# Performance work log

Hardware: AMD Instinct MI355X
Metric: run time of the kernel (lower is better)

## Reference

```python
import jax, jax.numpy as jnp
import numpy as np
from jax.ops import segment_sum, segment_max

N = 20000   # nodes per node type (glom, imm)
E = 320000  # edges per edge type (avg degree 16)
D = 256     # feature dim (in == out, required by GIN's (1+eps)*x + aggr)
LN_EPS = 1e-5


def _ln_relu(x, gamma, beta):
    mu = jnp.mean(x, axis=-1, keepdims=True)
    var = jnp.mean((x - mu) ** 2, axis=-1, keepdims=True)
    return jax.nn.relu((x - mu) * jax.lax.rsqrt(var + LN_EPS) * gamma + beta)


def _forward(x_glom, x_imm, ew_gg, ea_ig, W_gcn, b_gcn, Wl, bl, Wr, br, att, We,
             b_gat, eps, W_gin, b_gin, gamma, beta, ei_gg, ei_ig, ei_gi):
    # ---- GCNConv on (glom->glom): add_self_loops=True, edge_weight=ew_gg ----
    src, dst = ei_gg[0], ei_gg[1]
    xw = x_glom @ W_gcn                                   # [N, D]
    deg = segment_sum(ew_gg, dst, num_segments=N) + 1.0   # +1 for self-loop weight
    dinv = jax.lax.rsqrt(deg)                             # [N]
    coef = dinv[src] * ew_gg * dinv[dst]                  # [E] symmetric gcn_norm
    out_gcn = segment_sum(coef[:, None] * xw[src], dst, num_segments=N)
    out_gcn = out_gcn + (dinv * dinv)[:, None] * xw + b_gcn  # self-loop + bias

    # ---- GATv2Conv on (imm->glom): heads=1, edge_dim=1, no self loops ----
    s, d = ei_ig[0], ei_ig[1]
    hl = x_imm @ Wl + bl          # lin_l on source  [N, D]
    hr = x_glom @ Wr + br         # lin_r on target  [N, D]
    he = ea_ig @ We               # lin_edge         [E, D]
    z = jax.nn.leaky_relu(hl[s] + hr[d] + he, 0.2)
    logits = z @ att              # [E]
    m = segment_max(logits, d, num_segments=N)            # stable segment softmax
    ex = jnp.exp(logits - m[d])
    denom = segment_sum(ex, d, num_segments=N)
    alpha = ex / denom[d]
    out_gat = segment_sum(alpha[:, None] * hl[s], d, num_segments=N) + b_gat

    # ---- GINConv on (glom->imm): nn = Linear, train_eps ----
    s2, d2 = ei_gi[0], ei_gi[1]
    agg = segment_sum(x_glom[s2], d2, num_segments=N)     # sum aggregation
    out_gin = ((1.0 + eps[0]) * x_imm + agg) @ W_gin + b_gin

    # HeteroConv(aggr='sum') across edge types per destination node type,
    # then shared LayerNorm + ReLU
    glom = _ln_relu(out_gcn + out_gat, gamma, beta)
    imm = _ln_relu(out_gin, gamma, beta)
    return glom, imm


def setup_inputs() -> dict:
    key = jax.random.key(0)
    k = jax.random.split(key, 13)
    s = 0.06  # ~ glorot-ish scale for D=256
    return {
        'x_glom': jax.random.normal(k[0], (N, D), jnp.float32),
        'x_imm': jax.random.normal(k[1], (N, D), jnp.float32),
        'ew_gg': jax.random.uniform(k[2], (E,), jnp.float32),
        'ea_ig': jax.random.normal(k[3], (E, 1), jnp.float32),
        'W_gcn': jax.random.normal(k[4], (D, D), jnp.float32) * s,
        'b_gcn': jnp.zeros((D,), jnp.float32),
        'Wl': jax.random.normal(k[5], (D, D), jnp.float32) * s,
        'bl': jnp.zeros((D,), jnp.float32),
        'Wr': jax.random.normal(k[6], (D, D), jnp.float32) * s,
        'br': jnp.zeros((D,), jnp.float32),
        'att': jax.random.normal(k[7], (D,), jnp.float32) * s,
        'We': jax.random.normal(k[8], (1, D), jnp.float32) * s,
        'b_gat': jnp.zeros((D,), jnp.float32),
        'eps': jnp.zeros((1,), jnp.float32),
        'W_gin': jax.random.normal(k[9], (D, D), jnp.float32) * s,
        'b_gin': jnp.zeros((D,), jnp.float32),
        'gamma': jnp.ones((D,), jnp.float32),
        'beta': jnp.zeros((D,), jnp.float32),
        'ei_gg': jax.random.randint(k[10], (2, E), 0, N),
        'ei_ig': jax.random.randint(k[11], (2, E), 0, N),
        'ei_gi': jax.random.randint(k[12], (2, E), 0, N),
    }


def reference(x_glom, x_imm, ew_gg, ea_ig, W_gcn, b_gcn, Wl, bl, Wr, br, att, We,
              b_gat, eps, W_gin, b_gin, gamma, beta, ei_gg, ei_ig, ei_gi):
    return _forward(x_glom, x_imm, ew_gg, ea_ig, W_gcn, b_gcn, Wl, bl, Wr, br,
                    att, We, b_gat, eps, W_gin, b_gin, gamma, beta,
                    ei_gg, ei_ig, ei_gi)
```

## Files before the change

### kernel.cpp

```cpp
#include <hip/hip_runtime.h>


constexpr int D = 256;

typedef __attribute__((ext_vector_type(4))) float f32x4v;
typedef __attribute__((ext_vector_type(8))) short short8;

__device__ __forceinline__ float4 ld4(const float* p) {
    return *reinterpret_cast<const float4*>(p);
}
__device__ __forceinline__ void st4(float* p, float4 v) {
    *reinterpret_cast<float4*>(p) = v;
}
__device__ __forceinline__ unsigned short f2bf(float f) {
    unsigned u = __float_as_uint(f);
    u = u + 0x7FFFu + ((u >> 16) & 1u);
    return (unsigned short)(u >> 16);
}
__device__ __forceinline__ float bf2f(unsigned short u) {
    return __uint_as_float(((unsigned)u) << 16);
}
__device__ __forceinline__ float4 ldb4(const unsigned short* p) {
    ushort4 u = *reinterpret_cast<const ushort4*>(p);
    return make_float4(bf2f(u.x), bf2f(u.y), bf2f(u.z), bf2f(u.w));
}
__device__ __forceinline__ float wave_sum(float p) {
#pragma unroll
    for (int off = 32; off > 0; off >>= 1) p += __shfl_xor(p, off, 64);
    return p;
}
__device__ __forceinline__ float gat_partial(float4 h, float4 hrv, float ea,
                                             float4 We4, float4 att4) {
    float z, pp = 0.f;
    z = h.x + hrv.x + ea * We4.x; z *= (z > 0.f) ? 1.0f : 0.2f; pp += z * att4.x;
    z = h.y + hrv.y + ea * We4.y; z *= (z > 0.f) ? 1.0f : 0.2f; pp += z * att4.y;
    z = h.z + hrv.z + ea * We4.z; z *= (z > 0.f) ? 1.0f : 0.2f; pp += z * att4.z;
    z = h.w + hrv.w + ea * We4.w; z *= (z > 0.f) ? 1.0f : 0.2f; pp += z * att4.w;
    return pp;
}

__global__ void k_cast2(const float* __restrict__ x0, unsigned short* __restrict__ y0,
                        const float* __restrict__ x1, unsigned short* __restrict__ y1,
                        int n4)
{
    int i = blockIdx.x * 256 + threadIdx.x;
    if (i >= n4) return;
    const float* x = blockIdx.y ? x1 : x0;
    unsigned short* y = blockIdx.y ? y1 : y0;
    float4 v = ld4(x + (size_t)i * 4);
    ushort4 o;
    o.x = f2bf(v.x); o.y = f2bf(v.y); o.z = f2bf(v.z); o.w = f2bf(v.w);
    *reinterpret_cast<ushort4*>(y + (size_t)i * 4) = o;
}

__global__ void k_prep_wtz(const float* __restrict__ W0, const float* __restrict__ W1,
                           const float* __restrict__ W2, const float* __restrict__ W3,
                           unsigned short* __restrict__ Wt, int* __restrict__ counts,
                           float* __restrict__ deg, int n3, int N)
{
    int w = blockIdx.y;
    int i = blockIdx.x * 256 + threadIdx.x;
    if (w < 4) {
        const float* W = (w == 0) ? W0 : (w == 1) ? W1 : (w == 2) ? W2 : W3;
        int c = i >> 8, k = i & 255;
        Wt[(size_t)w * D * D + i] = f2bf(W[k * D + c]);
    } else {
        if (i < n3) counts[i] = 0;
        if (i < N) deg[i] = 1.0f;
    }
}

__global__ __launch_bounds__(256)
void k_proj(const unsigned short* __restrict__ xbg,
            const unsigned short* __restrict__ xbi,
            const unsigned short* __restrict__ Wt,
            const float* __restrict__ deg,
            const float* __restrict__ br, const float* __restrict__ bl,
            unsigned short* __restrict__ xws, unsigned short* __restrict__ hr,
            unsigned short* __restrict__ hl, int M)
{
    const int lane = threadIdx.x & 63;
    const int wave = threadIdx.x >> 6;
    const int lr = lane & 15;
    const int lk = lane >> 4;
    const int yy = blockIdx.y;
    const int row0 = blockIdx.x * 256 + wave * 64;

    const unsigned short* A;
    const unsigned short* Bt0;
    int col0;
    if (yy < 8) { A = xbg; Bt0 = Wt;             col0 = yy * 64; }
    else        { A = xbi; Bt0 = Wt + 2 * D * D; col0 = (yy - 8) * 64; }

    const unsigned short* ap[4];
#pragma unroll
    for (int rf = 0; rf < 4; ++rf) {
        int arow = row0 + rf * 16 + lr;
        int arow_c = (arow < M) ? arow : (M - 1);
        ap[rf] = A + (size_t)arow_c * D + lk * 8;
    }
    const unsigned short* bp = Bt0 + (size_t)(col0 + lr) * D + lk * 8;

    f32x4v acc[4][4] = {};
#pragma unroll
    for (int k0 = 0; k0 < 256; k0 += 32) {
        short8 af[4], bf[4];
#pragma unroll
        for (int rf = 0; rf < 4; ++rf)
            af[rf] = *reinterpret_cast<const short8*>(ap[rf] + k0);
#pragma unroll
        for (int nf = 0; nf < 4; ++nf)
            bf[nf] = *reinterpret_cast<const short8*>(bp + (size_t)nf * 16 * D + k0);
#pragma unroll
        for (int rf = 0; rf < 4; ++rf)
#pragma unroll
            for (int nf = 0; nf < 4; ++nf)
                acc[rf][nf] = __builtin_amdgcn_mfma_f32_16x16x32_bf16(
                    af[rf], bf[nf], acc[rf][nf], 0, 0, 0);
    }

#pragma unroll
    for (int nf = 0; nf < 4; ++nf) {
        int c = col0 + nf * 16 + lr;
        unsigned short* dst;
        int cc;
        float bv;
        bool scaled;
        if (yy < 8) {
            if (c < 256) { dst = xws; cc = c;       bv = 0.f;    scaled = true;  }
            else         { dst = hr;  cc = c - 256; bv = br[cc]; scaled = false; }
        } else           { dst = hl;  cc = c;       bv = bl[cc]; scaled = false; }
#pragma unroll
        for (int rf = 0; rf < 4; ++rf) {
#pragma unroll
            for (int i = 0; i < 4; ++i) {
                int r = row0 + rf * 16 + 4 * lk + i;
                if (r < M) {
                    float sc = scaled ? rsqrtf(deg[r]) : 1.0f;
                    dst[(size_t)r * D + cc] = f2bf(acc[rf][nf][i] * sc + bv);
                }
            }
        }
    }
}

__global__ __launch_bounds__(256)
void k_gin_gemm_ln(const unsigned short* __restrict__ A,
                   const unsigned short* __restrict__ Bt,
                   const float* __restrict__ bias,
                   const float* __restrict__ gamma, const float* __restrict__ beta,
                   float* __restrict__ out, int M)
{
    __shared__ float lds_s[4][64];
    __shared__ float lds_q[4][64];
    const int lane = threadIdx.x & 63;
    const int wave = threadIdx.x >> 6;
    const int lr = lane & 15;
    const int lk = lane >> 4;
    const int row0 = blockIdx.x * 64;
    const int col0 = wave * 64;

    const unsigned short* ap[4];
#pragma unroll
    for (int rf = 0; rf < 4; ++rf) {
        int arow = row0 + rf * 16 + lr;
        int arow_c = (arow < M) ? arow : (M - 1);
        ap[rf] = A + (size_t)arow_c * D + lk * 8;
    }
    const unsigned short* bp = Bt + (size_t)(col0 + lr) * D + lk * 8;

    f32x4v acc[4][4] = {};
#pragma unroll
    for (int k0 = 0; k0 < 256; k0 += 32) {
        short8 af[4], bf[4];
#pragma unroll
        for (int rf = 0; rf < 4; ++rf)
            af[rf] = *reinterpret_cast<const short8*>(ap[rf] + k0);
#pragma unroll
        for (int nf = 0; nf < 4; ++nf)
            bf[nf] = *reinterpret_cast<const short8*>(bp + (size_t)nf * 16 * D + k0);
#pragma unroll
        for (int rf = 0; rf < 4; ++rf)
#pragma unroll
            for (int nf = 0; nf < 4; ++nf)
                acc[rf][nf] = __builtin_amdgcn_mfma_f32_16x16x32_bf16(
                    af[rf], bf[nf], acc[rf][nf], 0, 0, 0);
    }

    float bv[4], gv[4], be[4];
#pragma unroll
    for (int nf = 0; nf < 4; ++nf) {
        int c = col0 + nf * 16 + lr;
        bv[nf] = bias[c]; gv[nf] = gamma[c]; be[nf] = beta[c];
    }

#pragma unroll
    for (int rf = 0; rf < 4; ++rf) {
        float ps[4], pq[4];
#pragma unroll
        for (int i = 0; i < 4; ++i) {
            float s = 0.f, q = 0.f;
#pragma unroll
            for (int nf = 0; nf < 4; ++nf) {
                float v = acc[rf][nf][i] + bv[nf];
                acc[rf][nf][i] = v;
                s += v; q += v * v;
            }
            ps[i] = s; pq[i] = q;
        }
#pragma unroll
        for (int off = 1; off < 16; off <<= 1) {
#pragma unroll
            for (int i = 0; i < 4; ++i) {
                ps[i] += __shfl_xor(ps[i], off, 64);
                pq[i] += __shfl_xor(pq[i], off, 64);
            }
        }
        if (lr == 0) {
#pragma unroll
            for (int i = 0; i < 4; ++i) {
                lds_s[wave][rf * 16 + lk * 4 + i] = ps[i];
                lds_q[wave][rf * 16 + lk * 4 + i] = pq[i];
            }
        }
    }
    __syncthreads();

#pragma unroll
    for (int rf = 0; rf < 4; ++rf) {
#pragma unroll
        for (int i = 0; i < 4; ++i) {
            int rl = rf * 16 + 4 * lk + i;
            float s = lds_s[0][rl] + lds_s[1][rl] + lds_s[2][rl] + lds_s[3][rl];
            float q = lds_q[0][rl] + lds_q[1][rl] + lds_q[2][rl] + lds_q[3][rl];
            float mu  = s * (1.0f / 256.0f);
            float var = q * (1.0f / 256.0f) - mu * mu;
            float rs  = rsqrtf(var + 1e-5f);
            int r = row0 + rl;
            if (r < M) {
#pragma unroll
                for (int nf = 0; nf < 4; ++nf) {
                    out[(size_t)r * D + col0 + nf * 16 + lr] =
                        fmaxf(0.f, (acc[rf][nf][i] - mu) * rs * gv[nf] + be[nf]);
                }
            }
        }
    }
}

__global__ void k_hist3(const int* __restrict__ ei_gg, const int* __restrict__ ei_ig,
                        const int* __restrict__ ei_gi, const float* __restrict__ ew_gg,
                        int* __restrict__ counts, int* __restrict__ rank,
                        float* __restrict__ deg, int E, int N)
{
    int e = blockIdx.x * 256 + threadIdx.x;
    if (e >= E) return;
    int t = blockIdx.y;
    const int* ei = (t == 0) ? ei_gg : (t == 1) ? ei_ig : ei_gi;
    int d = ei[E + e];
    rank[(size_t)t * E + e] = atomicAdd(&counts[t * N + d], 1);
    if (t == 0) atomicAdd(&deg[d], ew_gg[e]);
}

__global__ __launch_bounds__(256)
void k_scan_tile(const int* __restrict__ counts, int* __restrict__ rows,
                 int* __restrict__ partials, int N, int TPT)
{
    int t = blockIdx.y, tile = blockIdx.x;
    int i = tile * 256 + threadIdx.x;
    __shared__ int sh[256];
    int v = (i < N) ? counts[(size_t)t * N + i] : 0;
    sh[threadIdx.x] = v;
    __syncthreads();
#pragma unroll
    for (int off = 1; off < 256; off <<= 1) {
        int add = (threadIdx.x >= off) ? sh[threadIdx.x - off] : 0;
        __syncthreads();
        sh[threadIdx.x] += add;
        __syncthreads();
    }
    if (i < N) rows[(size_t)t * (N + 1) + i] = sh[threadIdx.x] - v;
    if (threadIdx.x == 255) partials[t * TPT + tile] = sh[255];
}

__global__ __launch_bounds__(128)
void k_scan_part(int* __restrict__ partials, int TPT)
{
    int t = blockIdx.x;
    __shared__ int sh[128];
    int v = (threadIdx.x < TPT) ? partials[t * TPT + threadIdx.x] : 0;
    sh[threadIdx.x] = v;
    __syncthreads();
#pragma unroll
    for (int off = 1; off < 128; off <<= 1) {
        int add = (threadIdx.x >= off) ? sh[threadIdx.x - off] : 0;
        __syncthreads();
        sh[threadIdx.x] += add;
        __syncthreads();
    }
    if (threadIdx.x < TPT) partials[t * TPT + threadIdx.x] = sh[threadIdx.x] - v;
}

__global__ void k_scan_final(int* __restrict__ rows, const int* __restrict__ partials,
                             int N, int TPT, int E)
{
    int i = blockIdx.x * 256 + threadIdx.x;
    if (i >= 3 * N) return;
    int t = i / N, j = i - t * N;
    rows[(size_t)t * (N + 1) + j] += partials[t * TPT + (j >> 8)];
    if (j == 0) rows[(size_t)t * (N + 1) + N] = E;
}

__global__ void k_scatter3(const int* __restrict__ ei_gg, const int* __restrict__ ei_ig,
                           const int* __restrict__ ei_gi, const float* __restrict__ ew_gg,
                           const float* __restrict__ ea_ig,
                           const int* __restrict__ rows, const int* __restrict__ rank,
                           int2* __restrict__ pk_gcn, int2* __restrict__ pk_gat,
                           int* __restrict__ src_gin, int E, int N)
{
    int e = blockIdx.x * 256 + threadIdx.x;
    if (e >= E) return;
    int t = blockIdx.y;
    if (t == 0) {
        int s = ei_gg[e], d = ei_gg[E + e];
        int pos = rows[d] + rank[e];
        pk_gcn[pos] = make_int2(s, __float_as_int(ew_gg[e]));
    } else if (t == 1) {
        int s = ei_ig[e], d = ei_ig[E + e];
        int pos = rows[(N + 1) + d] + rank[(size_t)E + e];
        pk_gat[pos] = make_int2(s, __float_as_int(ea_ig[e]));
    } else {
        int s = ei_gi[e], d = ei_gi[E + e];
        int pos = rows[2 * (N + 1) + d] + rank[2 * (size_t)E + e];
        src_gin[pos] = s;
    }
}

__global__ __launch_bounds__(256)
void k_gather_fused(const unsigned short* __restrict__ xws,
                    const unsigned short* __restrict__ hl,
                    const unsigned short* __restrict__ hr,
                    const float* __restrict__ deg,
                    const int* __restrict__ rows_gcn, const int2* __restrict__ pk_gcn,
                    const int* __restrict__ rows_gat, const int2* __restrict__ pk_gat,
                    const float* __restrict__ We, const float* __restrict__ att,
                    const float* __restrict__ b_gcn, const float* __restrict__ b_gat,
                    const float* __restrict__ gamma, const float* __restrict__ beta,
                    float* __restrict__ glom_out,
                    const unsigned short* __restrict__ xb_glom,
                    const float* __restrict__ x_imm, const float* __restrict__ eps,
                    const int* __restrict__ rows_gin, const int* __restrict__ src_gin,
                    unsigned short* __restrict__ agg,
                    int N)
{
    int gw   = __builtin_amdgcn_readfirstlane((blockIdx.x * 256 + threadIdx.x) >> 6);
    int lane = threadIdx.x & 63;

    if (gw < N) {
        int node = gw;
        float4 We4  = ld4(&We[lane * 4]);
        float4 att4 = ld4(&att[lane * 4]);
        float4 hrv  = ldb4(&hr[(size_t)node * D + lane * 4]);

        float di = rsqrtf(deg[node]);
        float4 acc = ldb4(&xws[(size_t)node * D + lane * 4]);
        float4 g0  = ld4(&b_gcn[lane * 4]);
        float4 a0  = ld4(&b_gat[lane * 4]);
        acc.x = di * acc.x + g0.x + a0.x;
        acc.y = di * acc.y + g0.y + a0.y;
        acc.z = di * acc.z + g0.z + a0.z;
        acc.w = di * acc.w + g0.w + a0.w;

        int p  = rows_gcn[node];
        int p1 = rows_gcn[node + 1];
        for (; p + 4 <= p1; p += 4) {
            int2  pk[4];
            float cf[4];
            float4 v[4];
#pragma unroll
            for (int j = 0; j < 4; ++j) pk[j] = pk_gcn[p + j];
#pragma unroll
            for (int j = 0; j < 4; ++j) cf[j] = __int_as_float(pk[j].y) * di;
#pragma unroll
            for (int j = 0; j < 4; ++j) v[j] = ldb4(&xws[(size_t)pk[j].x * D + lane * 4]);
#pragma unroll
            for (int j = 0; j < 4; ++j) {
                acc.x += cf[j] * v[j].x; acc.y += cf[j] * v[j].y;
                acc.z += cf[j] * v[j].z; acc.w += cf[j] * v[j].w;
            }
        }
        for (; p < p1; ++p) {
            int2 pk = pk_gcn[p];
            float cx = __int_as_float(pk.y) * di;
            float4 v = ldb4(&xws[(size_t)pk.x * D + lane * 4]);
            acc.x += cx * v.x; acc.y += cx * v.y;
            acc.z += cx * v.z; acc.w += cx * v.w;
        }

        int q  = rows_gat[node];
        int q1 = rows_gat[node + 1];
        int has = (q1 > q);
        float m = -3.4e38f, den = 0.f;
        float4 ag = make_float4(0.f, 0.f, 0.f, 0.f);
        for (; q + 4 <= q1; q += 4) {
            int2  pk[4];
            float4 h[4];
            float pp[4];
#pragma unroll
            for (int j = 0; j < 4; ++j) pk[j] = pk_gat[q + j];
#pragma unroll
            for (int j = 0; j < 4; ++j) h[j] = ldb4(&hl[(size_t)pk[j].x * D + lane * 4]);
#pragma unroll
            for (int j = 0; j < 4; ++j)
                pp[j] = wave_sum(gat_partial(h[j], hrv, __int_as_float(pk[j].y), We4, att4));
            float mb = fmaxf(fmaxf(pp[0], pp[1]), fmaxf(pp[2], pp[3]));
            float mn = fmaxf(m, mb);
            float scale = __expf(m - mn);
            float x[4];
#pragma unroll
            for (int j = 0; j < 4; ++j) x[j] = __expf(pp[j] - mn);
            den = den * scale + (x[0] + x[1]) + (x[2] + x[3]);
            float axx = 0.f, ayy = 0.f, azz = 0.f, aww = 0.f;
#pragma unroll
            for (int j = 0; j < 4; ++j) {
                axx += x[j] * h[j].x; ayy += x[j] * h[j].y;
                azz += x[j] * h[j].z; aww += x[j] * h[j].w;
            }
            ag.x = ag.x * scale + axx; ag.y = ag.y * scale + ayy;
            ag.z = ag.z * scale + azz; ag.w = ag.w * scale + aww;
            m = mn;
        }
        for (; q < q1; ++q) {
            int2 pk = pk_gat[q];
            float4 h = ldb4(&hl[(size_t)pk.x * D + lane * 4]);
            float pp = wave_sum(gat_partial(h, hrv, __int_as_float(pk.y), We4, att4));
            float mn = fmaxf(m, pp);
            float scale = __expf(m - mn);
            float ex = __expf(pp - mn);
            den = den * scale + ex;
            ag.x = ag.x * scale + ex * h.x;
            ag.y = ag.y * scale + ex * h.y;
            ag.z = ag.z * scale + ex * h.z;
            ag.w = ag.w * scale + ex * h.w;
            m = mn;
        }
        if (has) {
            float inv = 1.0f / den;
            acc.x += ag.x * inv; acc.y += ag.y * inv;
            acc.z += ag.z * inv; acc.w += ag.w * inv;
        }

        float s_ = acc.x + acc.y + acc.z + acc.w;
        float sq = acc.x * acc.x + acc.y * acc.y + acc.z * acc.z + acc.w * acc.w;
#pragma unroll
        for (int off = 32; off > 0; off >>= 1) {
            s_ += __shfl_xor(s_, off, 64);
            sq += __shfl_xor(sq, off, 64);
        }
        float mu  = s_ * (1.0f / 256.0f);
        float var = sq * (1.0f / 256.0f) - mu * mu;
        float rs  = rsqrtf(var + 1e-5f);
        float4 g = ld4(&gamma[lane * 4]);
        float4 b = ld4(&beta[lane * 4]);
        float4 o;
        o.x = fmaxf(0.f, (acc.x - mu) * rs * g.x + b.x);
        o.y = fmaxf(0.f, (acc.y - mu) * rs * g.y + b.y);
        o.z = fmaxf(0.f, (acc.z - mu) * rs * g.z + b.z);
        o.w = fmaxf(0.f, (acc.w - mu) * rs * g.w + b.w);
        st4(&glom_out[(size_t)node * D + lane * 4], o);
    } else if (gw < 2 * N) {
        int node = gw - N;
        float c = 1.0f + eps[0];
        float4 acc = ld4(&x_imm[(size_t)node * D + lane * 4]);
        acc.x *= c; acc.y *= c; acc.z *= c; acc.w *= c;
        int p  = rows_gin[node];
        int p1 = rows_gin[node + 1];
        for (; p + 4 <= p1; p += 4) {
            int s[4];
            float4 v[4];
#pragma unroll
            for (int j = 0; j < 4; ++j) s[j] = src_gin[p + j];
#pragma unroll
            for (int j = 0; j < 4; ++j) v[j] = ldb4(&xb_glom[(size_t)s[j] * D + lane * 4]);
            acc.x += (v[0].x + v[1].x) + (v[2].x + v[3].x);
            acc.y += (v[0].y + v[1].y) + (v[2].y + v[3].y);
            acc.z += (v[0].z + v[1].z) + (v[2].z + v[3].z);
            acc.w += (v[0].w + v[1].w) + (v[2].w + v[3].w);
        }
        for (; p < p1; ++p) {
            int sx = src_gin[p];
            float4 v = ldb4(&xb_glom[(size_t)sx * D + lane * 4]);
            acc.x += v.x; acc.y += v.y; acc.z += v.z; acc.w += v.w;
        }
        ushort4 o;
        o.x = f2bf(acc.x); o.y = f2bf(acc.y); o.z = f2bf(acc.z); o.w = f2bf(acc.w);
        *reinterpret_cast<ushort4*>(agg + (size_t)node * D + lane * 4) = o;
    }
}

extern "C" void kernel_launch(void* const* d_in, const int* in_sizes, int n_in,
                              void* d_out, int out_size, void* d_ws, size_t ws_size,
                              hipStream_t stream)
{
    const float* x_glom = (const float*)d_in[0];
    const float* x_imm  = (const float*)d_in[1];
    const float* ew_gg  = (const float*)d_in[2];
    const float* ea_ig  = (const float*)d_in[3];
    const float* W_gcn  = (const float*)d_in[4];
    const float* b_gcn  = (const float*)d_in[5];
    const float* Wl     = (const float*)d_in[6];
    const float* bl     = (const float*)d_in[7];
    const float* Wr     = (const float*)d_in[8];
    const float* br     = (const float*)d_in[9];
    const float* att    = (const float*)d_in[10];
    const float* We     = (const float*)d_in[11];
    const float* b_gat  = (const float*)d_in[12];
    const float* eps    = (const float*)d_in[13];
    const float* W_gin  = (const float*)d_in[14];
    const float* b_gin  = (const float*)d_in[15];
    const float* gamma  = (const float*)d_in[16];
    const float* beta   = (const float*)d_in[17];
    const int*   ei_gg  = (const int*)d_in[18];
    const int*   ei_ig  = (const int*)d_in[19];
    const int*   ei_gi  = (const int*)d_in[20];

    const int N = in_sizes[0] / D;
    const int E = in_sizes[2];
    const size_t ND = (size_t)N * D;
    const int TPT = (N + 255) / 256;

    char* base = (char*)d_ws;
    size_t off = 0;
    auto alloc = [&](size_t bytes) {
        void* p = base + off;
        off = (off + bytes + 255) & ~(size_t)255;
        return p;
    };
    unsigned short* xb_glom = (unsigned short*)alloc(ND * 2);
    unsigned short* xb_imm  = (unsigned short*)alloc(ND * 2);
    unsigned short* xws_b   = (unsigned short*)alloc(ND * 2);
    unsigned short* hl_b    = (unsigned short*)alloc(ND * 2);
    unsigned short* hr_b    = (unsigned short*)alloc(ND * 2);
    unsigned short* agg_b   = (unsigned short*)alloc(ND * 2);
    unsigned short* Wt      = (unsigned short*)alloc(4 * D * D * 2);
    float* deg     = (float*)alloc(N * 4);
    int*   counts  = (int*)alloc(3 * (size_t)N * 4);
    int*   rows    = (int*)alloc(3 * (size_t)(N + 1) * 4);
    int*   parts   = (int*)alloc(3 * (size_t)TPT * 4);
    int*   rank    = (int*)alloc(3 * (size_t)E * 4);
    int2*  pk_gcn  = (int2*)alloc((size_t)E * 8);
    int2*  pk_gat  = (int2*)alloc((size_t)E * 8);
    int*   src_gin = (int*)alloc((size_t)E * 4);

    float* glom_out = (float*)d_out;
    float* imm_out  = (float*)d_out + ND;

    int nb_cast  = (int)((ND / 4 + 255) / 256);
    int nb_3n    = (3 * N + 255) / 256;
    int nb_e     = (E + 255) / 256;
    int nb_2nw   = (2 * N + 3) / 4;

    k_cast2<<<dim3(nb_cast, 2), 256, 0, stream>>>(x_glom, xb_glom, x_imm, xb_imm,
                                                  (int)(ND / 4));
    k_prep_wtz<<<dim3(256, 5), 256, 0, stream>>>(W_gcn, Wr, Wl, W_gin, Wt,
                                                 counts, deg, 3 * N, N);
    k_hist3<<<dim3(nb_e, 3), 256, 0, stream>>>(ei_gg, ei_ig, ei_gi, ew_gg,
                                               counts, rank, deg, E, N);
    k_scan_tile<<<dim3(TPT, 3), 256, 0, stream>>>(counts, rows, parts, N, TPT);
    k_scan_part<<<3, 128, 0, stream>>>(parts, TPT);
    k_scan_final<<<nb_3n, 256, 0, stream>>>(rows, parts, N, TPT, E);
    k_scatter3<<<dim3(nb_e, 3), 256, 0, stream>>>(ei_gg, ei_ig, ei_gi, ew_gg, ea_ig,
                                                  rows, rank, pk_gcn, pk_gat,
                                                  src_gin, E, N);
    k_proj<<<dim3((N + 255) / 256, 12), 256, 0, stream>>>(
        xb_glom, xb_imm, Wt, deg, br, bl, xws_b, hr_b, hl_b, N);
    k_gather_fused<<<nb_2nw, 256, 0, stream>>>(
        xws_b, hl_b, hr_b, deg,
        rows, pk_gcn,
        rows + (N + 1), pk_gat,
        We, att, b_gcn, b_gat, gamma, beta, glom_out,
        xb_glom, x_imm, eps,
        rows + 2 * (N + 1), src_gin, agg_b, N);
    k_gin_gemm_ln<<<(N + 63) / 64, 256, 0, stream>>>(
        agg_b, Wt + 3 * D * D, b_gin, gamma, beta, imm_out, N);
}
```

Before: 250.3 us.

## Merge front-end and projection/scatter kernels, memset counters, prefetch edge indices

Merges the cast, weight transpose and histogram kernels into one launch, and the projection GEMM and CSR scatter into another. This cuts the number of kernel launches and lets independent work run concurrently. The counter and degree init becomes a memset, and the degree is stored as a sum with the +1 applied at use. The gather loops now software-prefetch the next four edge records to hide index-load latency, at the cost of a few more registers.

Result: faster. 240.4 us (-3.9%).

```diff
diff --git a/kernel.cpp b/kernel.cpp
--- a/kernel.cpp
+++ b/kernel.cpp
@@ -39,227 +39,51 @@
     return pp;
 }
 
-__global__ void k_cast2(const float* __restrict__ x0, unsigned short* __restrict__ y0,
-                        const float* __restrict__ x1, unsigned short* __restrict__ y1,
-                        int n4)
-{
-    int i = blockIdx.x * 256 + threadIdx.x;
-    if (i >= n4) return;
-    const float* x = blockIdx.y ? x1 : x0;
-    unsigned short* y = blockIdx.y ? y1 : y0;
-    float4 v = ld4(x + (size_t)i * 4);
-    ushort4 o;
-    o.x = f2bf(v.x); o.y = f2bf(v.y); o.z = f2bf(v.z); o.w = f2bf(v.w);
-    *reinterpret_cast<ushort4*>(y + (size_t)i * 4) = o;
-}
-
-__global__ void k_prep_wtz(const float* __restrict__ W0, const float* __restrict__ W1,
-                           const float* __restrict__ W2, const float* __restrict__ W3,
-                           unsigned short* __restrict__ Wt, int* __restrict__ counts,
-                           float* __restrict__ deg, int n3, int N)
-{
-    int w = blockIdx.y;
-    int i = blockIdx.x * 256 + threadIdx.x;
-    if (w < 4) {
+__global__ __launch_bounds__(256)
+void k_front(const float* __restrict__ x_glom, const float* __restrict__ x_imm,
+             unsigned short* __restrict__ xb_glom, unsigned short* __restrict__ xb_imm,
+             const float* __restrict__ W0, const float* __restrict__ W1,
+             const float* __restrict__ W2, const float* __restrict__ W3,
+             unsigned short* __restrict__ Wt,
+             const int* __restrict__ ei_gg, const int* __restrict__ ei_ig,
+             const int* __restrict__ ei_gi, const float* __restrict__ ew_gg,
+             int* __restrict__ counts, int* __restrict__ rank,
+             float* __restrict__ degsum,
+             int n4, int nbCast, int nbHist, int E, int N)
+{
+    int bx = blockIdx.x;
+    if (bx < 2 * nbCast) {
+        bool second = (bx >= nbCast);
+        int i = (second ? bx - nbCast : bx) * 256 + threadIdx.x;
+        if (i < n4) {
+            const float* x = second ? x_imm : x_glom;
+            unsigned short* y = second ? xb_imm : xb_glom;
+            float4 v = ld4(x + (size_t)i * 4);
+            ushort4 o;
+            o.x = f2bf(v.x); o.y = f2bf(v.y); o.z = f2bf(v.z); o.w = f2bf(v.w);
+            *reinterpret_cast<ushort4*>(y + (size_t)i * 4) = o;
+        }
+        return;
+    }
+    bx -= 2 * nbCast;
+    if (bx < 1024) {
+        int w = bx >> 8;
+        int i = ((bx & 255) << 8) + threadIdx.x;
         const float* W = (w == 0) ? W0 : (w == 1) ? W1 : (w == 2) ? W2 : W3;
         int c = i >> 8, k = i & 255;
         Wt[(size_t)w * D * D + i] = f2bf(W[k * D + c]);
-    } else {
-        if (i < n3) counts[i] = 0;
-        if (i < N) deg[i] = 1.0f;
-    }
-}
-
-__global__ __launch_bounds__(256)
-void k_proj(const unsigned short* __restrict__ xbg,
-            const unsigned short* __restrict__ xbi,
-            const unsigned short* __restrict__ Wt,
-            const float* __restrict__ deg,
-            const float* __restrict__ br, const float* __restrict__ bl,
-            unsigned short* __restrict__ xws, unsigned short* __restrict__ hr,
-            unsigned short* __restrict__ hl, int M)
-{
-    const int lane = threadIdx.x & 63;
-    const int wave = threadIdx.x >> 6;
-    const int lr = lane & 15;
-    const int lk = lane >> 4;
-    const int yy = blockIdx.y;
-    const int row0 = blockIdx.x * 256 + wave * 64;
-
-    const unsigned short* A;
-    const unsigned short* Bt0;
-    int col0;
-    if (yy < 8) { A = xbg; Bt0 = Wt;             col0 = yy * 64; }
-    else        { A = xbi; Bt0 = Wt + 2 * D * D; col0 = (yy - 8) * 64; }
-
-    const unsigned short* ap[4];
-#pragma unroll
-    for (int rf = 0; rf < 4; ++rf) {
-        int arow = row0 + rf * 16 + lr;
-        int arow_c = (arow < M) ? arow : (M - 1);
-        ap[rf] = A + (size_t)arow_c * D + lk * 8;
-    }
-    const unsigned short* bp = Bt0 + (size_t)(col0 + lr) * D + lk * 8;
-
-    f32x4v acc[4][4] = {};
-#pragma unroll
-    for (int k0 = 0; k0 < 256; k0 += 32) {
-        short8 af[4], bf[4];
-#pragma unroll
-        for (int rf = 0; rf < 4; ++rf)
-            af[rf] = *reinterpret_cast<const short8*>(ap[rf] + k0);
-#pragma unroll
-        for (int nf = 0; nf < 4; ++nf)
-            bf[nf] = *reinterpret_cast<const short8*>(bp + (size_t)nf * 16 * D + k0);
-#pragma unroll
-        for (int rf = 0; rf < 4; ++rf)
-#pragma unroll
-            for (int nf = 0; nf < 4; ++nf)
-                acc[rf][nf] = __builtin_amdgcn_mfma_f32_16x16x32_bf16(
-                    af[rf], bf[nf], acc[rf][nf], 0, 0, 0);
-    }
-
-#pragma unroll
-    for (int nf = 0; nf < 4; ++nf) {
-        int c = col0 + nf * 16 + lr;
-        unsigned short* dst;
-        int cc;
-        float bv;
-        bool scaled;
-        if (yy < 8) {
-            if (c < 256) { dst = xws; cc = c;       bv = 0.f;    scaled = true;  }
-            else         { dst = hr;  cc = c - 256; bv = br[cc]; scaled = false; }
-        } else           { dst = hl;  cc = c;       bv = bl[cc]; scaled = false; }
-#pragma unroll
-        for (int rf = 0; rf < 4; ++rf) {
-#pragma unroll
-            for (int i = 0; i < 4; ++i) {
-                int r = row0 + rf * 16 + 4 * lk + i;
-                if (r < M) {
-                    float sc = scaled ? rsqrtf(deg[r]) : 1.0f;
-                    dst[(size_t)r * D + cc] = f2bf(acc[rf][nf][i] * sc + bv);
-                }
-            }
-        }
-    }
-}
-
-__global__ __launch_bounds__(256)
-void k_gin_gemm_ln(const unsigned short* __restrict__ A,
-                   const unsigned short* __restrict__ Bt,
-                   const float* __restrict__ bias,
-                   const float* __restrict__ gamma, const float* __restrict__ beta,
-                   float* __restrict__ out, int M)
-{
-    __shared__ float lds_s[4][64];
-    __shared__ float lds_q[4][64];
-    const int lane = threadIdx.x & 63;
-    const int wave = threadIdx.x >> 6;
-    const int lr = lane & 15;
-    const int lk = lane >> 4;
-    const int row0 = blockIdx.x * 64;
-    const int col0 = wave * 64;
-
-    const unsigned short* ap[4];
-#pragma unroll
-    for (int rf = 0; rf < 4; ++rf) {
-        int arow = row0 + rf * 16 + lr;
-        int arow_c = (arow < M) ? arow : (M - 1);
-        ap[rf] = A + (size_t)arow_c * D + lk * 8;
-    }
-    const unsigned short* bp = Bt + (size_t)(col0 + lr) * D + lk * 8;
-
-    f32x4v acc[4][4] = {};
-#pragma unroll
-    for (int k0 = 0; k0 < 256; k0 += 32) {
-        short8 af[4], bf[4];
-#pragma unroll
-        for (int rf = 0; rf < 4; ++rf)
-            af[rf] = *reinterpret_cast<const short8*>(ap[rf] + k0);
-#pragma unroll
-        for (int nf = 0; nf < 4; ++nf)
-            bf[nf] = *reinterpret_cast<const short8*>(bp + (size_t)nf * 16 * D + k0);
-#pragma unroll
-        for (int rf = 0; rf < 4; ++rf)
-#pragma unroll
-            for (int nf = 0; nf < 4; ++nf)
-                acc[rf][nf] = __builtin_amdgcn_mfma_f32_16x16x32_bf16(
-                    af[rf], bf[nf], acc[rf][nf], 0, 0, 0);
-    }
-
-    float bv[4], gv[4], be[4];
-#pragma unroll
-    for (int nf = 0; nf < 4; ++nf) {
-        int c = col0 + nf * 16 + lr;
-        bv[nf] = bias[c]; gv[nf] = gamma[c]; be[nf] = beta[c];
-    }
-
-#pragma unroll
-    for (int rf = 0; rf < 4; ++rf) {
-        float ps[4], pq[4];
-#pragma unroll
-        for (int i = 0; i < 4; ++i) {
-            float s = 0.f, q = 0.f;
-#pragma unroll
-            for (int nf = 0; nf < 4; ++nf) {
-                float v = acc[rf][nf][i] + bv[nf];
-                acc[rf][nf][i] = v;
-                s += v; q += v * v;
-            }
-            ps[i] = s; pq[i] = q;
-        }
-#pragma unroll
-        for (int off = 1; off < 16; off <<= 1) {
-#pragma unroll
-            for (int i = 0; i < 4; ++i) {
-                ps[i] += __shfl_xor(ps[i], off, 64);
-                pq[i] += __shfl_xor(pq[i], off, 64);
-            }
-        }
-        if (lr == 0) {
-#pragma unroll
-            for (int i = 0; i < 4; ++i) {
-                lds_s[wave][rf * 16 + lk * 4 + i] = ps[i];
-                lds_q[wave][rf * 16 + lk * 4 + i] = pq[i];
-            }
-        }
-    }
-    __syncthreads();
-
-#pragma unroll
-    for (int rf = 0; rf < 4; ++rf) {
-#pragma unroll
-        for (int i = 0; i < 4; ++i) {
-            int rl = rf * 16 + 4 * lk + i;
-            float s = lds_s[0][rl] + lds_s[1][rl] + lds_s[2][rl] + lds_s[3][rl];
-            float q = lds_q[0][rl] + lds_q[1][rl] + lds_q[2][rl] + lds_q[3][rl];
-            float mu  = s * (1.0f / 256.0f);
-            float var = q * (1.0f / 256.0f) - mu * mu;
-            float rs  = rsqrtf(var + 1e-5f);
-            int r = row0 + rl;
-            if (r < M) {
-#pragma unroll
-                for (int nf = 0; nf < 4; ++nf) {
-                    out[(size_t)r * D + col0 + nf * 16 + lr] =
-                        fmaxf(0.f, (acc[rf][nf][i] - mu) * rs * gv[nf] + be[nf]);
-                }
-            }
-        }
-    }
-}
-
-__global__ void k_hist3(const int* __restrict__ ei_gg, const int* __restrict__ ei_ig,
-                        const int* __restrict__ ei_gi, const float* __restrict__ ew_gg,
-                        int* __restrict__ counts, int* __restrict__ rank,
-                        float* __restrict__ deg, int E, int N)
-{
-    int e = blockIdx.x * 256 + threadIdx.x;
-    if (e >= E) return;
-    int t = blockIdx.y;
-    const int* ei = (t == 0) ? ei_gg : (t == 1) ? ei_ig : ei_gi;
-    int d = ei[E + e];
-    rank[(size_t)t * E + e] = atomicAdd(&counts[t * N + d], 1);
-    if (t == 0) atomicAdd(&deg[d], ew_gg[e]);
+        return;
+    }
+    bx -= 1024;
+    {
+        int t = bx / nbHist;
+        int e = (bx - t * nbHist) * 256 + threadIdx.x;
+        if (e >= E) return;
+        const int* ei = (t == 0) ? ei_gg : (t == 1) ? ei_ig : ei_gi;
+        int d = ei[E + e];
+        rank[(size_t)t * E + e] = atomicAdd(&counts[t * N + d], 1);
+        if (t == 0) atomicAdd(&degsum[d], ew_gg[e]);
+    }
 }
 
 __global__ __launch_bounds__(256)
@@ -311,16 +135,95 @@
     if (j == 0) rows[(size_t)t * (N + 1) + N] = E;
 }
 
-__global__ void k_scatter3(const int* __restrict__ ei_gg, const int* __restrict__ ei_ig,
-                           const int* __restrict__ ei_gi, const float* __restrict__ ew_gg,
-                           const float* __restrict__ ea_ig,
-                           const int* __restrict__ rows, const int* __restrict__ rank,
-                           int2* __restrict__ pk_gcn, int2* __restrict__ pk_gat,
-                           int* __restrict__ src_gin, int E, int N)
-{
-    int e = blockIdx.x * 256 + threadIdx.x;
+__global__ __launch_bounds__(256)
+void k_mid(
+           const unsigned short* __restrict__ xbg,
+           const unsigned short* __restrict__ xbi,
+           const unsigned short* __restrict__ Wt,
+           const float* __restrict__ degsum,
+           const float* __restrict__ br, const float* __restrict__ bl,
+           unsigned short* __restrict__ xws, unsigned short* __restrict__ hr,
+           unsigned short* __restrict__ hl,
+           const int* __restrict__ ei_gg, const int* __restrict__ ei_ig,
+           const int* __restrict__ ei_gi, const float* __restrict__ ew_gg,
+           const float* __restrict__ ea_ig,
+           const int* __restrict__ rows, const int* __restrict__ rank,
+           int2* __restrict__ pk_gcn, int2* __restrict__ pk_gat,
+           int* __restrict__ src_gin,
+           int nbProjRow, int nbProj, int nbE, int E, int N, int M)
+{
+    int bx = blockIdx.x;
+    if (bx < nbProj) {
+        int brow = bx / 12;
+        int yy   = bx - brow * 12;
+        const int lane = threadIdx.x & 63;
+        const int wave = threadIdx.x >> 6;
+        const int lr = lane & 15;
+        const int lk = lane >> 4;
+        const int row0 = brow * 256 + wave * 64;
+
+        const unsigned short* A;
+        const unsigned short* Bt0;
+        int col0;
+        if (yy < 8) { A = xbg; Bt0 = Wt;             col0 = yy * 64; }
+        else        { A = xbi; Bt0 = Wt + 2 * D * D; col0 = (yy - 8) * 64; }
+
+        const unsigned short* ap[4];
+#pragma unroll
+        for (int rf = 0; rf < 4; ++rf) {
+            int arow = row0 + rf * 16 + lr;
+            int arow_c = (arow < M) ? arow : (M - 1);
+            ap[rf] = A + (size_t)arow_c * D + lk * 8;
+        }
+        const unsigned short* bp = Bt0 + (size_t)(col0 + lr) * D + lk * 8;
+
+        f32x4v acc[4][4] = {};
+#pragma unroll
+        for (int k0 = 0; k0 < 256; k0 += 32) {
+            short8 af[4], bf[4];
+#pragma unroll
+            for (int rf = 0; rf < 4; ++rf)
+                af[rf] = *reinterpret_cast<const short8*>(ap[rf] + k0);
+#pragma unroll
+            for (int nf = 0; nf < 4; ++nf)
+                bf[nf] = *reinterpret_cast<const short8*>(bp + (size_t)nf * 16 * D + k0);
+#pragma unroll
+            for (int rf = 0; rf < 4; ++rf)
+#pragma unroll
+                for (int nf = 0; nf < 4; ++nf)
+                    acc[rf][nf] = __builtin_amdgcn_mfma_f32_16x16x32_bf16(
+                        af[rf], bf[nf], acc[rf][nf], 0, 0, 0);
+        }
+
+#pragma unroll
+        for (int nf = 0; nf < 4; ++nf) {
+            int c = col0 + nf * 16 + lr;
+            unsigned short* dst;
+            int cc;
+            float bv;
+            bool scaled;
+            if (yy < 8) {
+                if (c < 256) { dst = xws; cc = c;       bv = 0.f;    scaled = true;  }
+                else         { dst = hr;  cc = c - 256; bv = br[cc]; scaled = false; }
+            } else           { dst = hl;  cc = c;       bv = bl[cc]; scaled = false; }
+#pragma unroll
+            for (int rf = 0; rf < 4; ++rf) {
+#pragma unroll
+                for (int i = 0; i < 4; ++i) {
+                    int r = row0 + rf * 16 + 4 * lk + i;
+                    if (r < M) {
+                        float sc = scaled ? rsqrtf(1.0f + degsum[r]) : 1.0f;
+                        dst[(size_t)r * D + cc] = f2bf(acc[rf][nf][i] * sc + bv);
+                    }
+                }
+            }
+        }
+        return;
+    }
+    int sx = bx - nbProj;
+    int t = sx / nbE;
+    int e = (sx - t * nbE) * 256 + threadIdx.x;
     if (e >= E) return;
-    int t = blockIdx.y;
     if (t == 0) {
         int s = ei_gg[e], d = ei_gg[E + e];
         int pos = rows[d] + rank[e];
@@ -337,10 +240,114 @@
 }
 
 __global__ __launch_bounds__(256)
+void k_gin_gemm_ln(const unsigned short* __restrict__ A,
+                   const unsigned short* __restrict__ Bt,
+                   const float* __restrict__ bias,
+                   const float* __restrict__ gamma, const float* __restrict__ beta,
+                   float* __restrict__ out, int M)
+{
+    __shared__ float lds_s[4][64];
+    __shared__ float lds_q[4][64];
+    const int lane = threadIdx.x & 63;
+    const int wave = threadIdx.x >> 6;
+    const int lr = lane & 15;
+    const int lk = lane >> 4;
+    const int row0 = blockIdx.x * 64;
+    const int col0 = wave * 64;
+
+    const unsigned short* ap[4];
+#pragma unroll
+    for (int rf = 0; rf < 4; ++rf) {
+        int arow = row0 + rf * 16 + lr;
+        int arow_c = (arow < M) ? arow : (M - 1);
+        ap[rf] = A + (size_t)arow_c * D + lk * 8;
+    }
+    const unsigned short* bp = Bt + (size_t)(col0 + lr) * D + lk * 8;
+
+    f32x4v acc[4][4] = {};
+#pragma unroll
+    for (int k0 = 0; k0 < 256; k0 += 32) {
+        short8 af[4], bf[4];
+#pragma unroll
+        for (int rf = 0; rf < 4; ++rf)
+            af[rf] = *reinterpret_cast<const short8*>(ap[rf] + k0);
+#pragma unroll
+        for (int nf = 0; nf < 4; ++nf)
+            bf[nf] = *reinterpret_cast<const short8*>(bp + (size_t)nf * 16 * D + k0);
+#pragma unroll
+        for (int rf = 0; rf < 4; ++rf)
+#pragma unroll
+            for (int nf = 0; nf < 4; ++nf)
+                acc[rf][nf] = __builtin_amdgcn_mfma_f32_16x16x32_bf16(
+                    af[rf], bf[nf], acc[rf][nf], 0, 0, 0);
+    }
+
+    float bv[4], gv[4], be[4];
+#pragma unroll
+    for (int nf = 0; nf < 4; ++nf) {
+        int c = col0 + nf * 16 + lr;
+        bv[nf] = bias[c]; gv[nf] = gamma[c]; be[nf] = beta[c];
+    }
+
+#pragma unroll
+    for (int rf = 0; rf < 4; ++rf) {
+        float ps[4], pq[4];
+#pragma unroll
+        for (int i = 0; i < 4; ++i) {
+            float s = 0.f, q = 0.f;
+#pragma unroll
+            for (int nf = 0; nf < 4; ++nf) {
+                float v = acc[rf][nf][i] + bv[nf];
+                acc[rf][nf][i] = v;
+                s += v; q += v * v;
+            }
+            ps[i] = s; pq[i] = q;
+        }
+#pragma unroll
+        for (int off = 1; off < 16; off <<= 1) {
+#pragma unroll
+            for (int i = 0; i < 4; ++i) {
+                ps[i] += __shfl_xor(ps[i], off, 64);
+                pq[i] += __shfl_xor(pq[i], off, 64);
+            }
+        }
+        if (lr == 0) {
+#pragma unroll
+            for (int i = 0; i < 4; ++i) {
+                lds_s[wave][rf * 16 + lk * 4 + i] = ps[i];
+                lds_q[wave][rf * 16 + lk * 4 + i] = pq[i];
+            }
+        }
+    }
+    __syncthreads();
+
+#pragma unroll
+    for (int rf = 0; rf < 4; ++rf) {
+#pragma unroll
+        for (int i = 0; i < 4; ++i) {
+            int rl = rf * 16 + 4 * lk + i;
+            float s = lds_s[0][rl] + lds_s[1][rl] + lds_s[2][rl] + lds_s[3][rl];
+            float q = lds_q[0][rl] + lds_q[1][rl] + lds_q[2][rl] + lds_q[3][rl];
+            float mu  = s * (1.0f / 256.0f);
+            float var = q * (1.0f / 256.0f) - mu * mu;
+            float rs  = rsqrtf(var + 1e-5f);
+            int r = row0 + rl;
+            if (r < M) {
+#pragma unroll
+                for (int nf = 0; nf < 4; ++nf) {
+                    out[(size_t)r * D + col0 + nf * 16 + lr] =
+                        fmaxf(0.f, (acc[rf][nf][i] - mu) * rs * gv[nf] + be[nf]);
+                }
+            }
+        }
+    }
+}
+
+__global__ __launch_bounds__(256)
 void k_gather_fused(const unsigned short* __restrict__ xws,
                     const unsigned short* __restrict__ hl,
                     const unsigned short* __restrict__ hr,
-                    const float* __restrict__ deg,
+                    const float* __restrict__ degsum,
                     const int* __restrict__ rows_gcn, const int2* __restrict__ pk_gcn,
                     const int* __restrict__ rows_gat, const int2* __restrict__ pk_gat,
                     const float* __restrict__ We, const float* __restrict__ att,
@@ -362,7 +369,7 @@
         float4 att4 = ld4(&att[lane * 4]);
         float4 hrv  = ldb4(&hr[(size_t)node * D + lane * 4]);
 
-        float di = rsqrtf(deg[node]);
+        float di = rsqrtf(1.0f + degsum[node]);
         float4 acc = ldb4(&xws[(size_t)node * D + lane * 4]);
         float4 g0  = ld4(&b_gcn[lane * 4]);
         float4 a0  = ld4(&b_gat[lane * 4]);
@@ -373,16 +380,26 @@
 
         int p  = rows_gcn[node];
         int p1 = rows_gcn[node + 1];
-        for (; p + 4 <= p1; p += 4) {
-            int2  pk[4];
+        int2 pkn[4];
+        if (p + 4 <= p1) {
+#pragma unroll
+            for (int j = 0; j < 4; ++j) pkn[j] = pk_gcn[p + j];
+        }
+        while (p + 4 <= p1) {
+            int2 pkc[4];
+#pragma unroll
+            for (int j = 0; j < 4; ++j) pkc[j] = pkn[j];
+            p += 4;
+            if (p + 4 <= p1) {
+#pragma unroll
+                for (int j = 0; j < 4; ++j) pkn[j] = pk_gcn[p + j];
+            }
             float cf[4];
             float4 v[4];
 #pragma unroll
-            for (int j = 0; j < 4; ++j) pk[j] = pk_gcn[p + j];
-#pragma unroll
-            for (int j = 0; j < 4; ++j) cf[j] = __int_as_float(pk[j].y) * di;
-#pragma unroll
-            for (int j = 0; j < 4; ++j) v[j] = ldb4(&xws[(size_t)pk[j].x * D + lane * 4]);
+            for (int j = 0; j < 4; ++j) cf[j] = __int_as_float(pkc[j].y) * di;
+#pragma unroll
+            for (int j = 0; j < 4; ++j) v[j] = ldb4(&xws[(size_t)pkc[j].x * D + lane * 4]);
 #pragma unroll
             for (int j = 0; j < 4; ++j) {
                 acc.x += cf[j] * v[j].x; acc.y += cf[j] * v[j].y;
@@ -402,17 +419,27 @@
         int has = (q1 > q);
         float m = -3.4e38f, den = 0.f;
         float4 ag = make_float4(0.f, 0.f, 0.f, 0.f);
-        for (; q + 4 <= q1; q += 4) {
-            int2  pk[4];
+        int2 qkn[4];
+        if (q + 4 <= q1) {
+#pragma unroll
+            for (int j = 0; j < 4; ++j) qkn[j] = pk_gat[q + j];
+        }
+        while (q + 4 <= q1) {
+            int2 qkc[4];
+#pragma unroll
+            for (int j = 0; j < 4; ++j) qkc[j] = qkn[j];
+            q += 4;
+            if (q + 4 <= q1) {
+#pragma unroll
+                for (int j = 0; j < 4; ++j) qkn[j] = pk_gat[q + j];
+            }
             float4 h[4];
             float pp[4];
 #pragma unroll
-            for (int j = 0; j < 4; ++j) pk[j] = pk_gat[q + j];
-#pragma unroll
-            for (int j = 0; j < 4; ++j) h[j] = ldb4(&hl[(size_t)pk[j].x * D + lane * 4]);
+            for (int j = 0; j < 4; ++j) h[j] = ldb4(&hl[(size_t)qkc[j].x * D + lane * 4]);
 #pragma unroll
             for (int j = 0; j < 4; ++j)
-                pp[j] = wave_sum(gat_partial(h[j], hrv, __int_as_float(pk[j].y), We4, att4));
+                pp[j] = wave_sum(gat_partial(h[j], hrv, __int_as_float(qkc[j].y), We4, att4));
             float mb = fmaxf(fmaxf(pp[0], pp[1]), fmaxf(pp[2], pp[3]));
             float mn = fmaxf(m, mb);
             float scale = __expf(m - mn);
@@ -475,13 +502,23 @@
         acc.x *= c; acc.y *= c; acc.z *= c; acc.w *= c;
         int p  = rows_gin[node];
         int p1 = rows_gin[node + 1];
-        for (; p + 4 <= p1; p += 4) {
-            int s[4];
+        int sn[4];
+        if (p + 4 <= p1) {
+#pragma unroll
+            for (int j = 0; j < 4; ++j) sn[j] = src_gin[p + j];
+        }
+        while (p + 4 <= p1) {
+            int sc[4];
+#pragma unroll
+            for (int j = 0; j < 4; ++j) sc[j] = sn[j];
+            p += 4;
+            if (p + 4 <= p1) {
+#pragma unroll
+                for (int j = 0; j < 4; ++j) sn[j] = src_gin[p + j];
+            }
             float4 v[4];
 #pragma unroll
-            for (int j = 0; j < 4; ++j) s[j] = src_gin[p + j];
-#pragma unroll
-            for (int j = 0; j < 4; ++j) v[j] = ldb4(&xb_glom[(size_t)s[j] * D + lane * 4]);
+            for (int j = 0; j < 4; ++j) v[j] = ldb4(&xb_glom[(size_t)sc[j] * D + lane * 4]);
             acc.x += (v[0].x + v[1].x) + (v[2].x + v[3].x);
             acc.y += (v[0].y + v[1].y) + (v[2].y + v[3].y);
             acc.z += (v[0].z + v[1].z) + (v[2].z + v[3].z);
@@ -543,8 +580,8 @@
     unsigned short* hr_b    = (unsigned short*)alloc(ND * 2);
     unsigned short* agg_b   = (unsigned short*)alloc(ND * 2);
     unsigned short* Wt      = (unsigned short*)alloc(4 * D * D * 2);
-    float* deg     = (float*)alloc(N * 4);
-    int*   counts  = (int*)alloc(3 * (size_t)N * 4);
+    int*   counts  = (int*)alloc(3 * (size_t)N * 4 + (size_t)N * 4);
+    float* degsum  = (float*)(counts + 3 * (size_t)N);
     int*   rows    = (int*)alloc(3 * (size_t)(N + 1) * 4);
     int*   parts   = (int*)alloc(3 * (size_t)TPT * 4);
     int*   rank    = (int*)alloc(3 * (size_t)E * 4);
@@ -555,27 +592,30 @@
     float* glom_out = (float*)d_out;
     float* imm_out  = (float*)d_out + ND;
 
-    int nb_cast  = (int)((ND / 4 + 255) / 256);
-    int nb_3n    = (3 * N + 255) / 256;
-    int nb_e     = (E + 255) / 256;
-    int nb_2nw   = (2 * N + 3) / 4;
-
-    k_cast2<<<dim3(nb_cast, 2), 256, 0, stream>>>(x_glom, xb_glom, x_imm, xb_imm,
-                                                  (int)(ND / 4));
-    k_prep_wtz<<<dim3(256, 5), 256, 0, stream>>>(W_gcn, Wr, Wl, W_gin, Wt,
-                                                 counts, deg, 3 * N, N);
-    k_hist3<<<dim3(nb_e, 3), 256, 0, stream>>>(ei_gg, ei_ig, ei_gi, ew_gg,
-                                               counts, rank, deg, E, N);
+    const int n4      = (int)(ND / 4);
+    const int nbCast  = (n4 + 255) / 256;
+    const int nbHist  = (E + 255) / 256;
+    const int nb_3n   = (3 * N + 255) / 256;
+    const int nb_2nw  = (2 * N + 3) / 4;
+    const int nbProjRow = (N + 255) / 256;
+    const int nbProj    = nbProjRow * 12;
+
+    hipMemsetAsync(counts, 0, 4 * (size_t)N * 4, stream);
+    k_front<<<2 * nbCast + 1024 + 3 * nbHist, 256, 0, stream>>>(
+        x_glom, x_imm, xb_glom, xb_imm,
+        W_gcn, Wr, Wl, W_gin, Wt,
+        ei_gg, ei_ig, ei_gi, ew_gg,
+        counts, rank, degsum, n4, nbCast, nbHist, E, N);
     k_scan_tile<<<dim3(TPT, 3), 256, 0, stream>>>(counts, rows, parts, N, TPT);
     k_scan_part<<<3, 128, 0, stream>>>(parts, TPT);
     k_scan_final<<<nb_3n, 256, 0, stream>>>(rows, parts, N, TPT, E);
-    k_scatter3<<<dim3(nb_e, 3), 256, 0, stream>>>(ei_gg, ei_ig, ei_gi, ew_gg, ea_ig,
-                                                  rows, rank, pk_gcn, pk_gat,
-                                                  src_gin, E, N);
-    k_proj<<<dim3((N + 255) / 256, 12), 256, 0, stream>>>(
-        xb_glom, xb_imm, Wt, deg, br, bl, xws_b, hr_b, hl_b, N);
+    k_mid<<<nbProj + 3 * nbHist, 256, 0, stream>>>(
+        xb_glom, xb_imm, Wt, degsum, br, bl, xws_b, hr_b, hl_b,
+        ei_gg, ei_ig, ei_gi, ew_gg, ea_ig,
+        rows, rank, pk_gcn, pk_gat, src_gin,
+        nbProjRow, nbProj, nbHist, E, N, N);
     k_gather_fused<<<nb_2nw, 256, 0, stream>>>(
-        xws_b, hl_b, hr_b, deg,
+        xws_b, hl_b, hr_b, degsum,
         rows, pk_gcn,
         rows + (N + 1), pk_gat,
         We, att, b_gcn, b_gat, gamma, beta, glom_out,
```
